# Kernel optimization log

Hardware: AMD Instinct MI355X
Metric: run time of the kernel (lower is better)

Reference implementation:

```python
import jax, jax.numpy as jnp
import numpy as np
import math

B, T, C = 4, 2048, 1024
H = 16  # parallelAttentionPathways
D = C // H  # head dim = 64


def setup_inputs() -> dict:
    key = jax.random.key(0)
    k1, k2, k3 = jax.random.split(key, 3)
    x = jax.random.normal(k1, (B, T, C), dtype=jnp.float32)
    w_qkv = jax.random.normal(k2, (3 * C, C), dtype=jnp.float32) * (1.0 / math.sqrt(C))
    w_out = jax.random.normal(k3, (C, C), dtype=jnp.float32) * (1.0 / math.sqrt(C))
    return {"x": x, "w_qkv": w_qkv, "w_out": w_out}


def reference(x, w_qkv, w_out):
    b, t, c = x.shape
    # qkv projection: torch Linear y = x @ W^T (no bias)
    qkv = jnp.einsum('btc,fc->btf', x, w_qkv)  # [B,T,3C]
    q, k, v = jnp.split(qkv, 3, axis=-1)
    # [B,H,T,D]
    q = q.reshape(b, t, H, D).transpose(0, 2, 1, 3)
    k = k.reshape(b, t, H, D).transpose(0, 2, 1, 3)
    v = v.reshape(b, t, H, D).transpose(0, 2, 1, 3)
    scale = 1.0 / math.sqrt(D)
    att = jnp.einsum('bhqd,bhkd->bhqk', q, k) * scale  # [B,H,T,T]
    causal = jnp.tril(jnp.ones((t, t), dtype=bool))
    att = jnp.where(causal[None, None], att, -jnp.inf)
    att = jax.nn.softmax(att, axis=-1)
    # dropoutRate=0.0 -> dropout is identity (eval-mode determinism)
    y = jnp.einsum('bhqk,bhkd->bhqd', att, v)  # [B,H,T,D]
    y = y.transpose(0, 2, 1, 3).reshape(b, t, c)
    return jnp.einsum('btc,fc->btf', y, w_out)
```

## Files before the change

### kernel.cpp

```cpp
#include <hip/hip_runtime.h>
#include <hip/hip_bf16.h>
#include <stdint.h>


using bf16 = __hip_bfloat16;
typedef __attribute__((ext_vector_type(8))) __bf16 bf16x8;
typedef __attribute__((ext_vector_type(8))) unsigned short u16x8;
typedef __attribute__((ext_vector_type(4))) unsigned short u16x4;
typedef __attribute__((ext_vector_type(4))) float f32x4;
typedef unsigned short ushort_t;

#define MFMA16(a, b, c) __builtin_amdgcn_mfma_f32_16x16x32_bf16((a), (b), (c), 0, 0, 0)

__device__ __forceinline__ bf16x8 ld_frag(const ushort_t* p) {
  const u16x8 u = *(const u16x8*)p;
  return __builtin_bit_cast(bf16x8, u);
}

__device__ __forceinline__ ushort_t f2bf(float f) {
  return __builtin_bit_cast(ushort_t, __float2bfloat16(f));
}

__device__ __forceinline__ void gl2lds16(const void* g, void* lds) {
  __builtin_amdgcn_global_load_lds((const __attribute__((address_space(1))) void*)g,
                                   (__attribute__((address_space(3))) void*)lds,
                                   16, 0, 0);
}

__global__ void detect_dtype(const ushort_t* __restrict__ x, int* __restrict__ flag) {
  __shared__ int red[256];
  const int tid = threadIdx.x;
  int cnt = 0;
  for (int i = tid; i < 4096; i += 256) {
    const int e = (x[i] & 0x7FFF) >> 7;
    cnt += (e >= 117 && e <= 133) ? 1 : 0;
  }
  red[tid] = cnt;
  __syncthreads();
  for (int s = 128; s > 0; s >>= 1) {
    if (tid < s) red[tid] += red[tid + s];
    __syncthreads();
  }
  if (tid == 0) *flag = (red[0] < 3072) ? 1 : 0;
}

__global__ void cvt_to_bf16(const void* __restrict__ in, ushort_t* __restrict__ out,
                            int n, const int* __restrict__ flag) {
  const int i = (blockIdx.x * 256 + threadIdx.x) * 8;
  if (i >= n) return;
  if (*flag) {
    const float* p = (const float*)in + i;
    const float4 f0 = *(const float4*)p;
    const float4 f1 = *(const float4*)(p + 4);
    u16x8 u;
    u[0] = f2bf(f0.x); u[1] = f2bf(f0.y); u[2] = f2bf(f0.z); u[3] = f2bf(f0.w);
    u[4] = f2bf(f1.x); u[5] = f2bf(f1.y); u[6] = f2bf(f1.z); u[7] = f2bf(f1.w);
    *(u16x8*)(out + i) = u;
  } else {
    *(u16x8*)(out + i) = *(const u16x8*)((const ushort_t*)in + i);
  }
}

template <int EPI>
__global__ __launch_bounds__(256, 2)
void gemm_nt(const ushort_t* __restrict__ A, const void* __restrict__ Bw,
             const int* __restrict__ flag, int bExt,
             float* __restrict__ C0, ushort_t* __restrict__ Qo,
             ushort_t* __restrict__ Ko, ushort_t* __restrict__ Vt,
             int M, int N, int Kd) {
  __shared__ ushort_t sA[128 * 32];
  __shared__ ushort_t sB[128 * 32];
  const int tid = threadIdx.x;
  const int wave = tid >> 6, lane = tid & 63;
  const int quad = lane >> 4, l16 = lane & 15;
  const int wm = wave >> 1, wn = wave & 1;
  const long m0 = (long)blockIdx.y * 128;
  const long n0 = (long)blockIdx.x * 128;
  const int bF = bExt ? *flag : 0;

  f32x4 acc[4][4];
#pragma unroll
  for (int i = 0; i < 4; ++i)
#pragma unroll
    for (int j = 0; j < 4; ++j) acc[i][j] = (f32x4){0.f, 0.f, 0.f, 0.f};

  for (int k0 = 0; k0 < Kd; k0 += 32) {
#pragma unroll
    for (int j = 0; j < 2; ++j) {
      const int chunk = wave * 2 + j;
      const int idx = chunk * 64 + lane;
      const int r = idx >> 2, c = idx & 3;
      gl2lds16(A + (m0 + r) * (long)Kd + k0 + c * 8, (char*)sA + chunk * 1024);
    }
    if (!bF) {
#pragma unroll
      for (int j = 0; j < 2; ++j) {
        const int chunk = wave * 2 + j;
        const int idx = chunk * 64 + lane;
        const int r = idx >> 2, c = idx & 3;
        gl2lds16((const ushort_t*)Bw + (n0 + r) * (long)Kd + k0 + c * 8,
                 (char*)sB + chunk * 1024);
      }
    } else {
#pragma unroll
      for (int t2 = 0; t2 < 2; ++t2) {
        const int idx = t2 * 256 + tid;
        const int r = idx >> 2, c = idx & 3;
        const float* p = (const float*)Bw + (n0 + r) * (long)Kd + k0 + c * 8;
        const float4 f0 = *(const float4*)p;
        const float4 f1 = *(const float4*)(p + 4);
        u16x8 u;
        u[0] = f2bf(f0.x); u[1] = f2bf(f0.y); u[2] = f2bf(f0.z); u[3] = f2bf(f0.w);
        u[4] = f2bf(f1.x); u[5] = f2bf(f1.y); u[6] = f2bf(f1.z); u[7] = f2bf(f1.w);
        *(u16x8*)&sB[r * 32 + c * 8] = u;
      }
    }
    __syncthreads();
    bf16x8 af[4], bfr[4];
#pragma unroll
    for (int i = 0; i < 4; ++i) {
      const int r = wm * 64 + i * 16 + l16;
      af[i] = ld_frag(&sA[r * 32 + quad * 8]);
    }
#pragma unroll
    for (int i = 0; i < 4; ++i) {
      const int r = wn * 64 + i * 16 + l16;
      bfr[i] = ld_frag(&sB[r * 32 + quad * 8]);
    }
#pragma unroll
    for (int i = 0; i < 4; ++i)
#pragma unroll
      for (int j = 0; j < 4; ++j) acc[i][j] = MFMA16(af[i], bfr[j], acc[i][j]);
    __syncthreads();
  }

#pragma unroll
  for (int i = 0; i < 4; ++i) {
#pragma unroll
    for (int j = 0; j < 4; ++j) {
      if (EPI == 0) {
#pragma unroll
        for (int reg = 0; reg < 4; ++reg) {
          const long m = m0 + wm * 64 + i * 16 + quad * 4 + reg;
          const long n = n0 + wn * 64 + j * 16 + l16;
          C0[m * N + n] = acc[i][j][reg];
        }
      } else {
        const long n = n0 + wn * 64 + j * 16 + l16;
        const int which = (int)(n >> 10);
        const int h = (int)((n >> 6) & 15);
        const int d = (int)(n & 63);
        const long mbase = m0 + wm * 64 + i * 16 + quad * 4;
        const long b = mbase >> 11;
        const long tb = mbase & 2047;
        if (which == 2) {
          u16x4 pk;
#pragma unroll
          for (int reg = 0; reg < 4; ++reg) pk[reg] = f2bf(acc[i][j][reg]);
          *(u16x4*)&Vt[((b * 16 + h) * 64 + d) * 2048 + tb] = pk;
        } else {
          ushort_t* dst = (which == 0) ? Qo : Ko;
#pragma unroll
          for (int reg = 0; reg < 4; ++reg)
            dst[((b * 16 + h) * 2048 + tb + reg) * 64 + d] = f2bf(acc[i][j][reg]);
        }
      }
    }
  }
}

#define RS 72

__device__ __forceinline__ void attn_tile(const bf16x8 qf[2], const ushort_t* sK,
                                          const ushort_t* sV, ushort_t* sPw,
                                          int kv, int qg, int quad, int l16,
                                          float& m_i, float& l_i, f32x4* oacc) {
  f32x4 s[4];
#pragma unroll
  for (int nt = 0; nt < 4; ++nt) s[nt] = (f32x4){0.f, 0.f, 0.f, 0.f};
#pragma unroll
  for (int nt = 0; nt < 4; ++nt) {
#pragma unroll
    for (int kk = 0; kk < 2; ++kk) {
      const bf16x8 kf = ld_frag(&sK[(nt * 16 + l16) * RS + (kk * 4 + quad) * 8]);
      s[nt] = MFMA16(kf, qf[kk], s[nt]);
    }
  }
  const int kb = kv * 64 + quad * 4;
  float rmax = -1e30f;
#pragma unroll
  for (int nt = 0; nt < 4; ++nt) {
#pragma unroll
    for (int reg = 0; reg < 4; ++reg) {
      float v = s[nt][reg] * 0.125f;
      if (kb + nt * 16 + reg > qg) v = -1e30f;
      s[nt][reg] = v;
      rmax = fmaxf(rmax, v);
    }
  }
  rmax = fmaxf(rmax, __shfl_xor(rmax, 16, 64));
  rmax = fmaxf(rmax, __shfl_xor(rmax, 32, 64));
  const float mnew = fmaxf(m_i, rmax);
  float rs = 0.f;
#pragma unroll
  for (int nt = 0; nt < 4; ++nt) {
#pragma unroll
    for (int reg = 0; reg < 4; ++reg) {
      const float p = __expf(s[nt][reg] - mnew);
      s[nt][reg] = p;
      rs += p;
    }
  }
  rs += __shfl_xor(rs, 16, 64);
  rs += __shfl_xor(rs, 32, 64);
  const float alpha = __expf(m_i - mnew);
  l_i = l_i * alpha + rs;
  m_i = mnew;
#pragma unroll
  for (int dt = 0; dt < 4; ++dt) oacc[dt] *= alpha;

  __threadfence_block();
#pragma unroll
  for (int nt = 0; nt < 4; ++nt) {
    u16x4 pk;
#pragma unroll
    for (int reg = 0; reg < 4; ++reg) pk[reg] = f2bf(s[nt][reg]);
    *(u16x4*)&sPw[l16 * RS + nt * 16 + quad * 4] = pk;
  }
  __threadfence_block();
  bf16x8 pf[2];
#pragma unroll
  for (int kk = 0; kk < 2; ++kk)
    pf[kk] = ld_frag(&sPw[l16 * RS + kk * 32 + quad * 8]);
#pragma unroll
  for (int dt = 0; dt < 4; ++dt) {
#pragma unroll
    for (int kk = 0; kk < 2; ++kk) {
      const bf16x8 vf = ld_frag(&sV[(dt * 16 + l16) * RS + (kk * 4 + quad) * 8]);
      oacc[dt] = MFMA16(vf, pf[kk], oacc[dt]);
    }
  }
}

__global__ __launch_bounds__(256, 4)
void attn_causal(const ushort_t* __restrict__ Qg, const ushort_t* __restrict__ Kg,
                 const ushort_t* __restrict__ Vt, ushort_t* __restrict__ Yg) {
  __shared__ ushort_t sK[64 * RS];
  __shared__ ushort_t sV[64 * RS];
  __shared__ ushort_t sPQ[64 * RS];
  const int tid = threadIdx.x;
  const int wave = tid >> 6, lane = tid & 63;
  const int quad = lane >> 4, l16 = lane & 15;
  const int qx = blockIdx.x, bh = blockIdx.y;
  const int qtA = qx, qtB = 31 - qx;
  const size_t base = (size_t)bh * 2048 * 64;
  ushort_t* sPw = sPQ + wave * 16 * RS;

  bf16x8 qfA[2], qfB[2];
#pragma unroll
  for (int tile = 0; tile < 2; ++tile) {
    const int qt = tile ? qtB : qtA;
#pragma unroll
    for (int t2 = 0; t2 < 2; ++t2) {
      const int idx = t2 * 256 + tid;
      const int r = idx >> 3, c = idx & 7;
      *(u16x8*)&sPQ[r * RS + c * 8] =
          *(const u16x8*)(Qg + base + (size_t)(qt * 64 + r) * 64 + c * 8);
    }
    __syncthreads();
#pragma unroll
    for (int kk = 0; kk < 2; ++kk) {
      const bf16x8 f = ld_frag(&sPQ[(wave * 16 + l16) * RS + (kk * 4 + quad) * 8]);
      if (tile) qfB[kk] = f; else qfA[kk] = f;
    }
    __syncthreads();
  }

  float mA = -1e30f, lA = 0.f, mB = -1e30f, lB = 0.f;
  f32x4 oA[4], oB[4];
#pragma unroll
  for (int dt = 0; dt < 4; ++dt) {
    oA[dt] = (f32x4){0.f, 0.f, 0.f, 0.f};
    oB[dt] = (f32x4){0.f, 0.f, 0.f, 0.f};
  }
  const int qgA = qtA * 64 + wave * 16 + l16;
  const int qgB = qtB * 64 + wave * 16 + l16;

  for (int kv = 0; kv <= qtB; ++kv) {
    __syncthreads();
#pragma unroll
    for (int t2 = 0; t2 < 2; ++t2) {
      const int idx = t2 * 256 + tid;
      const int r = idx >> 3, c = idx & 7;
      *(u16x8*)&sK[r * RS + c * 8] =
          *(const u16x8*)(Kg + base + (size_t)(kv * 64 + r) * 64 + c * 8);
      *(u16x8*)&sV[r * RS + c * 8] =
          *(const u16x8*)(Vt + base + (size_t)r * 2048 + kv * 64 + c * 8);
    }
    __syncthreads();
    attn_tile(qfB, sK, sV, sPw, kv, qgB, quad, l16, mB, lB, oB);
    if (kv <= qtA)
      attn_tile(qfA, sK, sV, sPw, kv, qgA, quad, l16, mA, lA, oA);
  }

  const int b = bh >> 4, h = bh & 15;
#pragma unroll
  for (int tile = 0; tile < 2; ++tile) {
    const int qt = tile ? qtB : qtA;
    const float linv = 1.f / (tile ? lB : lA);
    const f32x4* o = tile ? oB : oA;
    const int t = qt * 64 + wave * 16 + l16;
#pragma unroll
    for (int dt = 0; dt < 4; ++dt) {
      u16x4 pk;
#pragma unroll
      for (int reg = 0; reg < 4; ++reg) pk[reg] = f2bf(o[dt][reg] * linv);
      *(u16x4*)&Yg[(((size_t)b * 2048 + t) * 16 + h) * 64 + dt * 16 + quad * 4] = pk;
    }
  }
}

extern "C" void kernel_launch(void* const* d_in, const int* in_sizes, int n_in,
                              void* d_out, int out_size, void* d_ws, size_t ws_size,
                              hipStream_t stream) {
  const void* x = d_in[0];
  const void* w_qkv = d_in[1];
  const void* w_out = d_in[2];
  float* out = (float*)d_out;

  const size_t per = (size_t)4 * 16 * 2048 * 64;
  const size_t nwqkv = (size_t)3072 * 1024;
  const size_t nwout = (size_t)1024 * 1024;
  ushort_t* qws = (ushort_t*)d_ws;
  ushort_t* kws = qws + per;
  ushort_t* vTws = kws + per;
  ushort_t* xyws = vTws + per;
  ushort_t* wqkvb = xyws + per;
  ushort_t* woutb = wqkvb + nwqkv;
  int* flag = (int*)(woutb + nwout);
  const size_t need = (size_t)(4 * per + nwqkv + nwout) * 2 + 16;
  const bool pre = ws_size >= need;
  (void)in_sizes; (void)n_in; (void)out_size;

  dim3 blk(256);
  if (!pre) flag = (int*)(xyws + per);
  detect_dtype<<<1, 256, 0, stream>>>((const ushort_t*)x, flag);
  cvt_to_bf16<<<4096, 256, 0, stream>>>(x, xyws, (int)per, flag);
  if (pre) {
    cvt_to_bf16<<<1536, 256, 0, stream>>>(w_qkv, wqkvb, (int)nwqkv, flag);
    cvt_to_bf16<<<512, 256, 0, stream>>>(w_out, woutb, (int)nwout, flag);
    gemm_nt<1><<<dim3(24, 64), blk, 0, stream>>>(xyws, wqkvb, flag, 0, nullptr,
                                                 qws, kws, vTws, 8192, 3072, 1024);
    attn_causal<<<dim3(16, 64), blk, 0, stream>>>(qws, kws, vTws, xyws);
    gemm_nt<0><<<dim3(8, 64), blk, 0, stream>>>(xyws, woutb, flag, 0, out,
                                                nullptr, nullptr, nullptr,
                                                8192, 1024, 1024);
  } else {
    gemm_nt<1><<<dim3(24, 64), blk, 0, stream>>>(xyws, w_qkv, flag, 1, nullptr,
                                                 qws, kws, vTws, 8192, 3072, 1024);
    attn_causal<<<dim3(16, 64), blk, 0, stream>>>(qws, kws, vTws, xyws);
    gemm_nt<0><<<dim3(8, 64), blk, 0, stream>>>(xyws, w_out, flag, 1, out,
                                                nullptr, nullptr, nullptr,
                                                8192, 1024, 1024);
  }
}
```

Before: 281.4 us.

## Prefetch next K/V tile into registers and interleave both query tiles' MFMAs

The attention loop now loads the next K/V tile into registers while the current tile is being computed, instead of loading it and stalling before compute. Both query tiles (A and B) share each K/V fragment load, and their QK and PV MFMAs are interleaved so more independent matrix operations are in flight. A second P buffer in shared memory keeps the two tiles' probabilities separate. Softmax switches to the hardware exp2 with log2e folded into the scale. The cost is higher register and LDS use per block, which could reduce occupancy.

```diff
diff --git a/kernel.cpp b/kernel.cpp
--- a/kernel.cpp
+++ b/kernel.cpp
@@ -11,6 +11,8 @@
 typedef unsigned short ushort_t;
 
 #define MFMA16(a, b, c) __builtin_amdgcn_mfma_f32_16x16x32_bf16((a), (b), (c), 0, 0, 0)
+#define EXP2(x) __builtin_amdgcn_exp2f(x)
+#define SCL 0.1803368801f
 
 __device__ __forceinline__ bf16x8 ld_frag(const ushort_t* p) {
   const u16x8 u = *(const u16x8*)p;
@@ -19,6 +21,12 @@
 
 __device__ __forceinline__ ushort_t f2bf(float f) {
   return __builtin_bit_cast(ushort_t, __float2bfloat16(f));
+}
+
+__device__ __forceinline__ u16x4 pk4(const f32x4 v) {
+  u16x4 r;
+  r[0] = f2bf(v[0]); r[1] = f2bf(v[1]); r[2] = f2bf(v[2]); r[3] = f2bf(v[3]);
+  return r;
 }
 
 __device__ __forceinline__ void gl2lds16(const void* g, void* lds) {
@@ -154,10 +162,7 @@
         const long b = mbase >> 11;
         const long tb = mbase & 2047;
         if (which == 2) {
-          u16x4 pk;
-#pragma unroll
-          for (int reg = 0; reg < 4; ++reg) pk[reg] = f2bf(acc[i][j][reg]);
-          *(u16x4*)&Vt[((b * 16 + h) * 64 + d) * 2048 + tb] = pk;
+          *(u16x4*)&Vt[((b * 16 + h) * 64 + d) * 2048 + tb] = pk4(acc[i][j]);
         } else {
           ushort_t* dst = (which == 0) ? Qo : Ko;
 #pragma unroll
@@ -171,28 +176,15 @@
 
 #define RS 72
 
-__device__ __forceinline__ void attn_tile(const bf16x8 qf[2], const ushort_t* sK,
-                                          const ushort_t* sV, ushort_t* sPw,
-                                          int kv, int qg, int quad, int l16,
-                                          float& m_i, float& l_i, f32x4* oacc) {
-  f32x4 s[4];
-#pragma unroll
-  for (int nt = 0; nt < 4; ++nt) s[nt] = (f32x4){0.f, 0.f, 0.f, 0.f};
+__device__ __forceinline__ void softmax_upd(f32x4 s[4], int kb, int qg,
+                                            float& m_i, float& l_i, f32x4* oacc,
+                                            ushort_t* sPw, int quad, int l16) {
+  float rmax = -1e30f;
 #pragma unroll
   for (int nt = 0; nt < 4; ++nt) {
 #pragma unroll
-    for (int kk = 0; kk < 2; ++kk) {
-      const bf16x8 kf = ld_frag(&sK[(nt * 16 + l16) * RS + (kk * 4 + quad) * 8]);
-      s[nt] = MFMA16(kf, qf[kk], s[nt]);
-    }
-  }
-  const int kb = kv * 64 + quad * 4;
-  float rmax = -1e30f;
-#pragma unroll
-  for (int nt = 0; nt < 4; ++nt) {
-#pragma unroll
     for (int reg = 0; reg < 4; ++reg) {
-      float v = s[nt][reg] * 0.125f;
+      float v = s[nt][reg] * SCL;
       if (kb + nt * 16 + reg > qg) v = -1e30f;
       s[nt][reg] = v;
       rmax = fmaxf(rmax, v);
@@ -206,40 +198,21 @@
   for (int nt = 0; nt < 4; ++nt) {
 #pragma unroll
     for (int reg = 0; reg < 4; ++reg) {
-      const float p = __expf(s[nt][reg] - mnew);
+      const float p = EXP2(s[nt][reg] - mnew);
       s[nt][reg] = p;
       rs += p;
     }
   }
   rs += __shfl_xor(rs, 16, 64);
   rs += __shfl_xor(rs, 32, 64);
-  const float alpha = __expf(m_i - mnew);
+  const float alpha = EXP2(m_i - mnew);
   l_i = l_i * alpha + rs;
   m_i = mnew;
 #pragma unroll
   for (int dt = 0; dt < 4; ++dt) oacc[dt] *= alpha;
-
-  __threadfence_block();
-#pragma unroll
-  for (int nt = 0; nt < 4; ++nt) {
-    u16x4 pk;
-#pragma unroll
-    for (int reg = 0; reg < 4; ++reg) pk[reg] = f2bf(s[nt][reg]);
-    *(u16x4*)&sPw[l16 * RS + nt * 16 + quad * 4] = pk;
-  }
-  __threadfence_block();
-  bf16x8 pf[2];
-#pragma unroll
-  for (int kk = 0; kk < 2; ++kk)
-    pf[kk] = ld_frag(&sPw[l16 * RS + kk * 32 + quad * 8]);
-#pragma unroll
-  for (int dt = 0; dt < 4; ++dt) {
-#pragma unroll
-    for (int kk = 0; kk < 2; ++kk) {
-      const bf16x8 vf = ld_frag(&sV[(dt * 16 + l16) * RS + (kk * 4 + quad) * 8]);
-      oacc[dt] = MFMA16(vf, pf[kk], oacc[dt]);
-    }
-  }
+#pragma unroll
+  for (int nt = 0; nt < 4; ++nt)
+    *(u16x4*)&sPw[l16 * RS + nt * 16 + quad * 4] = pk4(s[nt]);
 }
 
 __global__ __launch_bounds__(256, 4)
@@ -248,13 +221,15 @@
   __shared__ ushort_t sK[64 * RS];
   __shared__ ushort_t sV[64 * RS];
   __shared__ ushort_t sPQ[64 * RS];
+  __shared__ ushort_t sPB[64 * RS];
   const int tid = threadIdx.x;
   const int wave = tid >> 6, lane = tid & 63;
   const int quad = lane >> 4, l16 = lane & 15;
   const int qx = blockIdx.x, bh = blockIdx.y;
   const int qtA = qx, qtB = 31 - qx;
   const size_t base = (size_t)bh * 2048 * 64;
-  ushort_t* sPw = sPQ + wave * 16 * RS;
+  ushort_t* sPwA = sPQ + wave * 16 * RS;
+  ushort_t* sPwB = sPB + wave * 16 * RS;
 
   bf16x8 qfA[2], qfB[2];
 #pragma unroll
@@ -286,21 +261,64 @@
   const int qgA = qtA * 64 + wave * 16 + l16;
   const int qgB = qtB * 64 + wave * 16 + l16;
 
+  const int r0 = tid >> 3, c0 = tid & 7;
+  const int r1 = (256 + tid) >> 3, c1 = tid & 7;
+  u16x8 rk0, rk1, rv0, rv1;
+  rk0 = *(const u16x8*)(Kg + base + (size_t)r0 * 64 + c0 * 8);
+  rk1 = *(const u16x8*)(Kg + base + (size_t)r1 * 64 + c1 * 8);
+  rv0 = *(const u16x8*)(Vt + base + (size_t)r0 * 2048 + c0 * 8);
+  rv1 = *(const u16x8*)(Vt + base + (size_t)r1 * 2048 + c1 * 8);
+
   for (int kv = 0; kv <= qtB; ++kv) {
     __syncthreads();
-#pragma unroll
-    for (int t2 = 0; t2 < 2; ++t2) {
-      const int idx = t2 * 256 + tid;
-      const int r = idx >> 3, c = idx & 7;
-      *(u16x8*)&sK[r * RS + c * 8] =
-          *(const u16x8*)(Kg + base + (size_t)(kv * 64 + r) * 64 + c * 8);
-      *(u16x8*)&sV[r * RS + c * 8] =
-          *(const u16x8*)(Vt + base + (size_t)r * 2048 + kv * 64 + c * 8);
-    }
-    __syncthreads();
-    attn_tile(qfB, sK, sV, sPw, kv, qgB, quad, l16, mB, lB, oB);
-    if (kv <= qtA)
-      attn_tile(qfA, sK, sV, sPw, kv, qgA, quad, l16, mA, lA, oA);
+    *(u16x8*)&sK[r0 * RS + c0 * 8] = rk0;
+    *(u16x8*)&sK[r1 * RS + c1 * 8] = rk1;
+    *(u16x8*)&sV[r0 * RS + c0 * 8] = rv0;
+    *(u16x8*)&sV[r1 * RS + c1 * 8] = rv1;
+    __syncthreads();
+    if (kv < qtB) {
+      const size_t kb2 = base + (size_t)(kv + 1) * 64 * 64;
+      rk0 = *(const u16x8*)(Kg + kb2 + (size_t)r0 * 64 + c0 * 8);
+      rk1 = *(const u16x8*)(Kg + kb2 + (size_t)r1 * 64 + c1 * 8);
+      rv0 = *(const u16x8*)(Vt + base + (size_t)r0 * 2048 + (kv + 1) * 64 + c0 * 8);
+      rv1 = *(const u16x8*)(Vt + base + (size_t)r1 * 2048 + (kv + 1) * 64 + c1 * 8);
+    }
+    const bool doA = (kv <= qtA);
+
+    f32x4 sb[4], sa[4];
+#pragma unroll
+    for (int nt = 0; nt < 4; ++nt) {
+      sb[nt] = (f32x4){0.f, 0.f, 0.f, 0.f};
+      sa[nt] = (f32x4){0.f, 0.f, 0.f, 0.f};
+    }
+#pragma unroll
+    for (int nt = 0; nt < 4; ++nt) {
+#pragma unroll
+      for (int kk = 0; kk < 2; ++kk) {
+        const bf16x8 kf = ld_frag(&sK[(nt * 16 + l16) * RS + (kk * 4 + quad) * 8]);
+        sb[nt] = MFMA16(kf, qfB[kk], sb[nt]);
+        if (doA) sa[nt] = MFMA16(kf, qfA[kk], sa[nt]);
+      }
+    }
+    const int kb = kv * 64 + quad * 4;
+    softmax_upd(sb, kb, qgB, mB, lB, oB, sPwB, quad, l16);
+    if (doA) softmax_upd(sa, kb, qgA, mA, lA, oA, sPwA, quad, l16);
+
+    bf16x8 pfB[2], pfA[2];
+#pragma unroll
+    for (int kk = 0; kk < 2; ++kk) {
+      pfB[kk] = ld_frag(&sPwB[l16 * RS + kk * 32 + quad * 8]);
+      if (doA) pfA[kk] = ld_frag(&sPwA[l16 * RS + kk * 32 + quad * 8]);
+    }
+#pragma unroll
+    for (int dt = 0; dt < 4; ++dt) {
+#pragma unroll
+      for (int kk = 0; kk < 2; ++kk) {
+        const bf16x8 vf = ld_frag(&sV[(dt * 16 + l16) * RS + (kk * 4 + quad) * 8]);
+        oB[dt] = MFMA16(vf, pfB[kk], oB[dt]);
+        if (doA) oA[dt] = MFMA16(vf, pfA[kk], oA[dt]);
+      }
+    }
   }
 
   const int b = bh >> 4, h = bh & 15;
@@ -312,10 +330,8 @@
     const int t = qt * 64 + wave * 16 + l16;
 #pragma unroll
     for (int dt = 0; dt < 4; ++dt) {
-      u16x4 pk;
-#pragma unroll
-      for (int reg = 0; reg < 4; ++reg) pk[reg] = f2bf(o[dt][reg] * linv);
-      *(u16x4*)&Yg[(((size_t)b * 2048 + t) * 16 + h) * 64 + dt * 16 + quad * 4] = pk;
+      const f32x4 v = o[dt] * linv;
+      *(u16x4*)&Yg[(((size_t)b * 2048 + t) * 16 + h) * 64 + dt * 16 + quad * 4] = pk4(v);
     }
   }
 }
```

Result: slower. 446.0 us (+58.5%).
